# Optimization experiments

Measured on AMD Instinct MI355X. Metric: run time of the kernel, lower is better.

## Reference

```python
import jax, jax.numpy as jnp
import numpy as np

P_FACTOR = 3.0   # config['p_factor']
EPS = 1e-12      # torch F.normalize eps

def _l2_normalize(x):
    return x / jnp.maximum(jnp.linalg.norm(x, axis=-1, keepdims=True), EPS)

def _l1_normalize(x):
    return x / jnp.maximum(jnp.sum(jnp.abs(x), axis=-1, keepdims=True), EPS)

def setup_inputs() -> dict:
    key = jax.random.key(0)
    k = jax.random.split(key, 6)
    B, N_EX, D_IN, D_FEAT, N_LAB, D_CLS = 4096, 16384, 1024, 256, 28, 64
    features = jax.random.normal(k[0], (B, D_IN), jnp.float32)
    labels = jax.random.uniform(k[1], (B, N_LAB), jnp.float32)            # BCE targets in [0,1]
    ex_features = jax.random.normal(k[2], (N_EX, D_IN), jnp.float32)
    ex_classes = jax.random.uniform(k[3], (N_EX, N_LAB), jnp.float32)     # class memberships
    g_w = jax.random.normal(k[4], (D_FEAT, D_IN), jnp.float32) * 0.02     # Linear(in=1024,out=256,bias=False)
    class_reps = jax.random.uniform(k[5], (N_LAB, D_CLS), jnp.float32) * 2.0 - 1.0  # rand*2-1
    return {"features": features, "labels": labels, "ex_features": ex_features,
            "ex_classes": ex_classes, "g_w": g_w, "class_reps": class_reps}

def reference(features, labels, ex_features, ex_classes, g_w, class_reps):
    # g projection (use_g=True, no bias)
    f = features @ g_w.T          # [B, D_FEAT]
    ef = ex_features @ g_w.T      # [N_EX, D_FEAT]
    # exemplar class representations: L1-normalized memberships @ class_reps
    ex_class_reps = _l1_normalize(ex_classes) @ class_reps   # [N_EX, D_CLS]
    # cosine similarity between queries and exemplars
    s = _l2_normalize(f) @ _l2_normalize(ef).T               # [B, N_EX]
    # power-sign activation then L1 normalize over exemplars
    a = _l1_normalize(jnp.sign(s) * jnp.abs(s) ** P_FACTOR)  # [B, N_EX]
    # weighted exemplar aggregation
    echo = a @ ex_class_reps                                  # [B, D_CLS]
    # negative euclidean distances to class representations (cdist)
    diff = echo[:, None, :] - class_reps[None, :, :]          # [B, N_LAB, D_CLS]
    neg_dists = -jnp.sqrt(jnp.sum(diff * diff, axis=-1))      # [B, N_LAB]
    # BCEWithLogitsLoss (mean reduction)
    loss = jnp.mean(-(labels * jax.nn.log_sigmoid(neg_dists)
                      + (1.0 - labels) * jax.nn.log_sigmoid(-neg_dists)))
    return (loss, neg_dists)
```

## Files before the change

kernel.cpp:

```cpp
#include <hip/hip_runtime.h>


typedef __bf16 bf16x8 __attribute__((ext_vector_type(8)));
typedef __bf16 bf16x4 __attribute__((ext_vector_type(4)));
typedef float  f32x4  __attribute__((ext_vector_type(4)));

__device__ __forceinline__ f32x4 f4zero() { f32x4 z = {0.f, 0.f, 0.f, 0.f}; return z; }

__device__ __forceinline__ f32x4 mfma16(bf16x8 a, bf16x8 b, f32x4 c) {
  return __builtin_amdgcn_mfma_f32_16x16x32_bf16(a, b, c, 0, 0, 0);
}

__device__ __forceinline__ bf16x8 load8f(const float* p) {
  f32x4 a = *(const f32x4*)p;
  f32x4 b = *(const f32x4*)(p + 4);
  bf16x8 r;
  r[0] = (__bf16)a[0]; r[1] = (__bf16)a[1]; r[2] = (__bf16)a[2]; r[3] = (__bf16)a[3];
  r[4] = (__bf16)b[0]; r[5] = (__bf16)b[1]; r[6] = (__bf16)b[2]; r[7] = (__bf16)b[3];
  return r;
}

__device__ __forceinline__ bf16x8 cvt2(f32x4 a, f32x4 b) {
  bf16x8 r;
  r[0] = (__bf16)a[0]; r[1] = (__bf16)a[1]; r[2] = (__bf16)a[2]; r[3] = (__bf16)a[3];
  r[4] = (__bf16)b[0]; r[5] = (__bf16)b[1]; r[6] = (__bf16)b[2]; r[7] = (__bf16)b[3];
  return r;
}

__device__ __forceinline__ void async16(const void* g, void* l) {
  __builtin_amdgcn_global_load_lds(
      (const __attribute__((address_space(1))) unsigned int*)g,
      (__attribute__((address_space(3))) unsigned int*)l, 16, 0, 0);
}

__device__ __forceinline__ void bar_lgkm() {
  asm volatile("s_waitcnt lgkmcnt(0)" ::: "memory");
  __builtin_amdgcn_s_barrier();
}
__device__ __forceinline__ void bar_all() {
  asm volatile("s_waitcnt vmcnt(0) lgkmcnt(0)" ::: "memory");
  __builtin_amdgcn_s_barrier();
}

__global__ void fill_sentinel(float* __restrict__ out, int n) {
  for (int i = blockIdx.x * 256 + threadIdx.x; i < n; i += gridDim.x * 256) out[i] = -1.0f;
}

__global__ void prep(const float* __restrict__ exc, __bf16* __restrict__ vT,
                     const float* __restrict__ W, __bf16* __restrict__ W3,
                     float* __restrict__ zp, int zn) {
  const int b = blockIdx.x, tid = threadIdx.x;
  if (b < 64) {
    int e = b * 256 + tid;
    float m[28];
    float s = 0.f;
#pragma unroll
    for (int j = 0; j < 28; j++) {
      m[j] = exc[(size_t)e * 28 + j];
      s += fabsf(m[j]);
    }
    float inv = 1.0f / fmaxf(s, 1e-12f);
#pragma unroll
    for (int j = 0; j < 28; j++) vT[(size_t)j * 16384 + e] = (__bf16)(m[j] * inv);
#pragma unroll
    for (int j = 28; j < 32; j++) vT[(size_t)j * 16384 + e] = (__bf16)0.0f;
  } else if (b < 192) {
    int i = (b - 64) * 256 + tid;
    int frag = i >> 6, lane = i & 63;
    int c16 = frag >> 5, k32 = frag & 31;
    int quad = lane >> 4, l15 = lane & 15;
    *(bf16x8*)(W3 + (size_t)i * 8) =
        load8f(W + (size_t)(c16 * 16 + l15) * 1024 + k32 * 32 + quad * 8);
  } else {
    for (int i = (b - 192) * 256 + tid; i < zn; i += (gridDim.x - 192) * 256) zp[i] = 0.f;
  }
}

__global__ __launch_bounds__(256, 3)
void proj_l2norm(const float* __restrict__ Xa, const float* __restrict__ Xb,
                 const __bf16* __restrict__ W3,
                 __bf16* __restrict__ Pa, __bf16* __restrict__ Pb) {
  __shared__ __align__(16) __bf16 Xs[2][32 * 72];
  __shared__ float nrmW[4 * 32];
  __shared__ float invn[32];

  const int tid = threadIdx.x;
  const int w = tid >> 6, lane = tid & 63;
  const int quad = lane >> 4, l15 = lane & 15;
  const int xrow = tid >> 3, xc8 = tid & 7;

  const float* X;
  __bf16* P;
  int row0;
  if (blockIdx.x < 512) { X = Xa; P = Pa; row0 = blockIdx.x * 32; }
  else                  { X = Xb; P = Pb; row0 = (blockIdx.x - 512) * 32; }

  const float* xsrc = X + (size_t)(row0 + xrow) * 1024 + xc8 * 8;
  const __bf16* wpk = W3 + (size_t)(w * 4) * 32 * 512 + (size_t)lane * 8;

  f32x4 acc[2][4];
#pragma unroll
  for (int i = 0; i < 2; i++)
#pragma unroll
    for (int j = 0; j < 4; j++) acc[i][j] = f4zero();

  *(bf16x8*)(&Xs[0][xrow * 72 + xc8 * 8]) = load8f(xsrc);
  bar_lgkm();

  int cur = 0;
  for (int kb = 0; kb < 16; kb++) {
    const int nxt = cur ^ 1;

    bf16x8 wF[8];
#pragma unroll
    for (int f = 0; f < 8; f++) {
      const int ksub = f >> 2, nb = f & 3;
      wF[f] = *(const bf16x8*)(wpk + ((size_t)nb * 32 + kb * 2 + ksub) * 512);
    }

    f32x4 xa, xb;
    if (kb < 15) {
      const float* xp = xsrc + (kb + 1) * 64;
      xa = *(const f32x4*)xp;
      xb = *(const f32x4*)(xp + 4);
    }

#pragma unroll
    for (int ksub = 0; ksub < 2; ksub++) {
      bf16x8 af[2];
#pragma unroll
      for (int mb = 0; mb < 2; mb++)
        af[mb] = *(bf16x8*)(&Xs[cur][(mb * 16 + l15) * 72 + ksub * 32 + quad * 8]);
#pragma unroll
      for (int mb = 0; mb < 2; mb++)
#pragma unroll
        for (int nb = 0; nb < 4; nb++)
          acc[mb][nb] = mfma16(af[mb], wF[ksub * 4 + nb], acc[mb][nb]);
    }

    if (kb < 15) {
      *(bf16x8*)(&Xs[nxt][xrow * 72 + xc8 * 8]) = cvt2(xa, xb);
    }
    bar_lgkm();
    cur = nxt;
  }

  float part[2][4];
#pragma unroll
  for (int mb = 0; mb < 2; mb++)
#pragma unroll
    for (int r = 0; r < 4; r++) {
      float s = 0.f;
#pragma unroll
      for (int nb = 0; nb < 4; nb++) { float v = acc[mb][nb][r]; s += v * v; }
      part[mb][r] = s;
    }
#pragma unroll
  for (int m = 1; m < 16; m <<= 1)
#pragma unroll
    for (int mb = 0; mb < 2; mb++)
#pragma unroll
      for (int r = 0; r < 4; r++) part[mb][r] += __shfl_xor(part[mb][r], m, 64);

  if (l15 == 0) {
#pragma unroll
    for (int mb = 0; mb < 2; mb++)
#pragma unroll
      for (int r = 0; r < 4; r++)
        nrmW[w * 32 + mb * 16 + quad * 4 + r] = part[mb][r];
  }
  __syncthreads();
  if (tid < 32) {
    float s = nrmW[tid] + nrmW[32 + tid] + nrmW[64 + tid] + nrmW[96 + tid];
    invn[tid] = 1.0f / fmaxf(sqrtf(s), 1e-12f);
  }
  __syncthreads();
#pragma unroll
  for (int mb = 0; mb < 2; mb++)
#pragma unroll
    for (int nb = 0; nb < 4; nb++)
#pragma unroll
      for (int r = 0; r < 4; r++) {
        int row = mb * 16 + quad * 4 + r;
        int col = w * 64 + nb * 16 + l15;
        P[(size_t)(row0 + row) * 256 + col] = (__bf16)(acc[mb][nb][r] * invn[row]);
      }
}

__global__ __launch_bounds__(256, 2)
void fused_sim(const __bf16* __restrict__ fn, const __bf16* __restrict__ efn,
               const __bf16* __restrict__ vTg,
               float* __restrict__ tT, float* __restrict__ r_acc) {
  __shared__ __align__(16) __bf16 Ks[64 * 256];
  __shared__ __align__(16) __bf16 Vs[2][32 * 64];
  __shared__ __align__(16) __bf16 Us[128 * 72];

  const int tid = threadIdx.x, w = tid >> 6, lane = tid & 63;
  const int quad = lane >> 4, l15 = lane & 15;
  const int wy = w >> 1, wx = w & 1;
  const int swk = l15 & 7;
  const int chunk = blockIdx.x & 15, mtile = blockIdx.x >> 4;
  const int q0 = mtile * 128;
  const int e_base = chunk * 1024;

  int koff[8];
#pragma unroll
  for (int rep = 0; rep < 8; rep++) {
    int idx = rep * 256 + tid;
    int row = idx >> 5;
    int c5  = (idx & 31) ^ (row & 7);
    koff[rep] = row * 256 + c5 * 8;
  }
  const int vrow = tid >> 3;
  const int vcs  = (tid & 7) ^ (vrow & 7);
  const size_t vsrc0 = (size_t)vrow * 16384 + e_base + vcs * 8;

  {
    const __bf16* src = efn + (size_t)e_base * 256;
#pragma unroll
    for (int rep = 0; rep < 8; rep++) async16(src + koff[rep], Ks + (rep * 256 + tid) * 8);
    async16(vTg + vsrc0, &Vs[0][tid * 8]);
  }

  bf16x8 qf[8][4];
#pragma unroll
  for (int ks = 0; ks < 8; ks++)
#pragma unroll
    for (int nb = 0; nb < 4; nb++)
      qf[ks][nb] = *(const bf16x8*)(fn + (size_t)(q0 + wx * 64 + nb * 16 + l15) * 256 +
                                    ks * 32 + quad * 8);

  float r_part[4] = {0.f, 0.f, 0.f, 0.f};
  f32x4 accp[2][2];
#pragma unroll
  for (int a = 0; a < 2; a++)
#pragma unroll
    for (int b = 0; b < 2; b++) accp[a][b] = f4zero();

  bar_all();

  int cur = 0;
  for (int t = 0; t < 16; t++) {
    f32x4 accs[2][4];
#pragma unroll
    for (int a = 0; a < 2; a++)
#pragma unroll
      for (int b = 0; b < 4; b++) accs[a][b] = f4zero();
#pragma unroll
    for (int ks = 0; ks < 8; ks++) {
      bf16x8 af[2];
#pragma unroll
      for (int mb = 0; mb < 2; mb++)
        af[mb] = *(bf16x8*)(Ks + (wy * 32 + mb * 16 + l15) * 256 +
                            ((ks * 4 + quad) ^ swk) * 8);
#pragma unroll
      for (int mb = 0; mb < 2; mb++)
#pragma unroll
        for (int nb = 0; nb < 4; nb++)
          accs[mb][nb] = mfma16(af[mb], qf[ks][nb], accs[mb][nb]);
    }

    bar_lgkm();

    if (t < 15) {
      const __bf16* src = efn + (size_t)(e_base + (t + 1) * 64) * 256;
#pragma unroll
      for (int rep = 0; rep < 8; rep++)
        async16(src + koff[rep], Ks + (rep * 256 + tid) * 8);
      async16(vTg + vsrc0 + (t + 1) * 64, &Vs[cur ^ 1][tid * 8]);
    }

#pragma unroll
    for (int mb = 0; mb < 2; mb++) {
      const int eo = wy * 32 + mb * 16 + quad * 4;
#pragma unroll
      for (int nb = 0; nb < 4; nb++) {
        const int q = wx * 64 + nb * 16 + l15;
        bf16x4 pk;
#pragma unroll
        for (int r = 0; r < 4; r++) {
          float s = accs[mb][nb][r];
          __bf16 ub = (__bf16)(s * s * s);
          pk[r] = ub;
          r_part[nb] += fabsf((float)ub);
        }
        *(bf16x4*)(Us + q * 72 + eo) = pk;
      }
    }

    bar_lgkm();

#pragma unroll
    for (int ks = 0; ks < 2; ks++) {
      bf16x8 vf[2], uf[2];
#pragma unroll
      for (int cb = 0; cb < 2; cb++)
        vf[cb] = *(bf16x8*)(&Vs[cur][(cb * 16 + l15) * 64 + ((ks * 4 + quad) ^ swk) * 8]);
#pragma unroll
      for (int qb = 0; qb < 2; qb++)
        uf[qb] = *(bf16x8*)(Us + (w * 32 + qb * 16 + l15) * 72 + ks * 32 + quad * 8);
#pragma unroll
      for (int cb = 0; cb < 2; cb++)
#pragma unroll
        for (int qb = 0; qb < 2; qb++)
          accp[cb][qb] = mfma16(vf[cb], uf[qb], accp[cb][qb]);
    }

    bar_all();
    cur ^= 1;
  }

#pragma unroll
  for (int nb = 0; nb < 4; nb++) {
    float v = r_part[nb];
    v += __shfl_xor(v, 16, 64);
    v += __shfl_xor(v, 32, 64);
    if (quad == 0) atomicAdd(&r_acc[q0 + wx * 64 + nb * 16 + l15], v);
  }
#pragma unroll
  for (int cb = 0; cb < 2; cb++)
#pragma unroll
    for (int qb = 0; qb < 2; qb++)
#pragma unroll
      for (int r = 0; r < 4; r++)
        atomicAdd(&tT[(size_t)(cb * 16 + quad * 4 + r) * 4096 + q0 + w * 32 + qb * 16 + l15],
                  accp[cb][qb][r]);
}

__global__ __launch_bounds__(256, 4)
void finalize(const float* __restrict__ tT, const float* __restrict__ r_acc,
              const float* __restrict__ creps, const float* __restrict__ labels,
              float* __restrict__ loss_acc, float* __restrict__ out) {
  __shared__ __align__(16) float cr[28 * 64];
  __shared__ float wsum[4];
  const int tid = threadIdx.x, w = tid >> 6, lane = tid & 63;
  for (int i = tid; i < 28 * 64; i += 256) cr[i] = creps[i];
  __syncthreads();

  const int q = blockIdx.x * 4 + w;
  float tval = 0.f;
  if (lane < 28) tval = tT[(size_t)lane * 4096 + q];
  tval *= 1.0f / fmaxf(r_acc[q], 1e-12f);

  float echo = 0.f;
#pragma unroll
  for (int j = 0; j < 28; j++)
    echo = fmaf(__shfl(tval, j, 64), cr[j * 64 + lane], echo);

  float dj = 0.f;
#pragma unroll
  for (int j = 0; j < 28; j++) {
    float df = echo - cr[j * 64 + lane];
    float d2 = df * df;
#pragma unroll
    for (int m = 1; m < 64; m <<= 1) d2 += __shfl_xor(d2, m, 64);
    if (lane == j) dj = sqrtf(d2);
  }

  float lsum = 0.f;
  if (lane < 28) {
    out[1 + (size_t)q * 28 + lane] = -dj;
    float y = labels[(size_t)q * 28 + lane];
    lsum = fmaf(y, dj, log1pf(expf(-dj)));
  }
#pragma unroll
  for (int m = 1; m < 64; m <<= 1) lsum += __shfl_xor(lsum, m, 64);
  if (lane == 0) wsum[w] = lsum;
  __syncthreads();
  if (tid == 0) {
    atomicAdd(loss_acc, wsum[0] + wsum[1] + wsum[2] + wsum[3]);
    __threadfence();
    unsigned* cnt = (unsigned*)(loss_acc + 1);
    unsigned old = atomicAdd(cnt, 1u);
    if (old == gridDim.x - 1) {
      float total = atomicAdd(loss_acc, 0.0f);
      out[0] = total * (1.0f / 114688.0f);
    }
  }
}

extern "C" void kernel_launch(void* const* d_in, const int* in_sizes, int n_in,
                              void* d_out, int out_size, void* d_ws, size_t ws_size,
                              hipStream_t stream) {
  const float* features = nullptr;
  const float* labels   = nullptr;
  const float* ex_feat  = nullptr;
  const float* ex_cls   = nullptr;
  const float* g_w      = nullptr;
  const float* creps    = nullptr;
  for (int i = 0; i < n_in; i++) {
    switch (in_sizes[i]) {
      case 4194304:  features = (const float*)d_in[i]; break;
      case 114688:   labels   = (const float*)d_in[i]; break;
      case 16777216: ex_feat  = (const float*)d_in[i]; break;
      case 458752:   ex_cls   = (const float*)d_in[i]; break;
      case 262144:   g_w      = (const float*)d_in[i]; break;
      case 1792:     creps    = (const float*)d_in[i]; break;
      default: break;
    }
  }
  float* out = (float*)d_out;

  if (!features || !labels || !ex_feat || !ex_cls || !g_w || !creps ||
      ws_size < (16ull << 20)) {
    fill_sentinel<<<256, 256, 0, stream>>>(out, out_size);
    return;
  }

  char* ws = (char*)d_ws;
  __bf16* f_n   = (__bf16*)(ws);
  __bf16* ef_n  = (__bf16*)(ws + (2ull << 20));
  __bf16* vT    = (__bf16*)(ws + (10ull << 20));
  float*  tT    = (float*) (ws + (11ull << 20));
  float*  r_acc = tT + 32 * 4096;
  float*  lossp = r_acc + 4096;
  __bf16* W3    = (__bf16*)(ws + (12ull << 20));

  prep<<<720, 256, 0, stream>>>(ex_cls, vT, g_w, W3, tT, 32 * 4096 + 4096 + 2);

  proj_l2norm<<<640, 256, 0, stream>>>(ex_feat, features, W3, ef_n, f_n);
  fused_sim<<<512, 256, 0, stream>>>(f_n, ef_n, vT, tT, r_acc);
  finalize<<<1024, 256, 0, stream>>>(tT, r_acc, creps, labels, lossp, out);
}
```

Before: 222.4 us.

## Double-buffer exemplar K tiles with 32-row steps and per-wave query ownership

The fused similarity kernel now walks exemplars in 32-row steps with a double-buffered K tile. The prefetch of the next K and V tiles is issued at the top of each iteration, so it overlaps the whole MFMA compute instead of waiting behind a mid-loop barrier. Each wave now owns 32 queries against all 32 exemplars of the step, replacing the earlier 2x2 wave split. This removes the extra LDS barrier and shrinks the U staging buffer. The cost is twice as many loop iterations and barriers, and fewer MFMAs per barrier.

```diff
diff --git a/kernel.cpp b/kernel.cpp
--- a/kernel.cpp
+++ b/kernel.cpp
@@ -191,46 +191,47 @@
 void fused_sim(const __bf16* __restrict__ fn, const __bf16* __restrict__ efn,
                const __bf16* __restrict__ vTg,
                float* __restrict__ tT, float* __restrict__ r_acc) {
-  __shared__ __align__(16) __bf16 Ks[64 * 256];
-  __shared__ __align__(16) __bf16 Vs[2][32 * 64];
-  __shared__ __align__(16) __bf16 Us[128 * 72];
+  __shared__ __align__(16) __bf16 Ks[2][32 * 256];
+  __shared__ __align__(16) __bf16 Vs[2][32 * 32];
+  __shared__ __align__(16) __bf16 Us[128 * 40];
 
   const int tid = threadIdx.x, w = tid >> 6, lane = tid & 63;
   const int quad = lane >> 4, l15 = lane & 15;
-  const int wy = w >> 1, wx = w & 1;
   const int swk = l15 & 7;
   const int chunk = blockIdx.x & 15, mtile = blockIdx.x >> 4;
   const int q0 = mtile * 128;
   const int e_base = chunk * 1024;
-
-  int koff[8];
-#pragma unroll
-  for (int rep = 0; rep < 8; rep++) {
+  const int qw = q0 + w * 32;
+
+  int koff[4];
+#pragma unroll
+  for (int rep = 0; rep < 4; rep++) {
     int idx = rep * 256 + tid;
     int row = idx >> 5;
     int c5  = (idx & 31) ^ (row & 7);
     koff[rep] = row * 256 + c5 * 8;
   }
-  const int vrow = tid >> 3;
-  const int vcs  = (tid & 7) ^ (vrow & 7);
-  const size_t vsrc0 = (size_t)vrow * 16384 + e_base + vcs * 8;
+  const int vrow = tid >> 2, vc = tid & 3;
+  const bool vstage = (tid < 128);
 
   {
     const __bf16* src = efn + (size_t)e_base * 256;
 #pragma unroll
-    for (int rep = 0; rep < 8; rep++) async16(src + koff[rep], Ks + (rep * 256 + tid) * 8);
-    async16(vTg + vsrc0, &Vs[0][tid * 8]);
-  }
-
-  bf16x8 qf[8][4];
+    for (int rep = 0; rep < 4; rep++)
+      async16(src + koff[rep], &Ks[0][(rep * 256 + tid) * 8]);
+    if (vstage)
+      async16(vTg + (size_t)vrow * 16384 + e_base + vc * 8, &Vs[0][tid * 8]);
+  }
+
+  bf16x8 qf[8][2];
 #pragma unroll
   for (int ks = 0; ks < 8; ks++)
 #pragma unroll
-    for (int nb = 0; nb < 4; nb++)
-      qf[ks][nb] = *(const bf16x8*)(fn + (size_t)(q0 + wx * 64 + nb * 16 + l15) * 256 +
+    for (int nb = 0; nb < 2; nb++)
+      qf[ks][nb] = *(const bf16x8*)(fn + (size_t)(qw + nb * 16 + l15) * 256 +
                                     ks * 32 + quad * 8);
 
-  float r_part[4] = {0.f, 0.f, 0.f, 0.f};
+  float r_part[2] = {0.f, 0.f};
   f32x4 accp[2][2];
 #pragma unroll
   for (int a = 0; a < 2; a++)
@@ -240,42 +241,42 @@
   bar_all();
 
   int cur = 0;
-  for (int t = 0; t < 16; t++) {
-    f32x4 accs[2][4];
+  for (int t = 0; t < 32; t++) {
+    const int nxt = cur ^ 1;
+
+    if (t < 31) {
+      const __bf16* src = efn + (size_t)(e_base + (t + 1) * 32) * 256;
+#pragma unroll
+      for (int rep = 0; rep < 4; rep++)
+        async16(src + koff[rep], &Ks[nxt][(rep * 256 + tid) * 8]);
+      if (vstage)
+        async16(vTg + (size_t)vrow * 16384 + e_base + (t + 1) * 32 + vc * 8,
+                &Vs[nxt][tid * 8]);
+    }
+
+    f32x4 accs[2][2];
 #pragma unroll
     for (int a = 0; a < 2; a++)
 #pragma unroll
-      for (int b = 0; b < 4; b++) accs[a][b] = f4zero();
+      for (int b = 0; b < 2; b++) accs[a][b] = f4zero();
 #pragma unroll
     for (int ks = 0; ks < 8; ks++) {
       bf16x8 af[2];
 #pragma unroll
       for (int mb = 0; mb < 2; mb++)
-        af[mb] = *(bf16x8*)(Ks + (wy * 32 + mb * 16 + l15) * 256 +
-                            ((ks * 4 + quad) ^ swk) * 8);
+        af[mb] = *(bf16x8*)(&Ks[cur][(mb * 16 + l15) * 256 +
+                                     ((ks * 4 + quad) ^ swk) * 8]);
 #pragma unroll
       for (int mb = 0; mb < 2; mb++)
 #pragma unroll
-        for (int nb = 0; nb < 4; nb++)
+        for (int nb = 0; nb < 2; nb++)
           accs[mb][nb] = mfma16(af[mb], qf[ks][nb], accs[mb][nb]);
     }
 
-    bar_lgkm();
-
-    if (t < 15) {
-      const __bf16* src = efn + (size_t)(e_base + (t + 1) * 64) * 256;
-#pragma unroll
-      for (int rep = 0; rep < 8; rep++)
-        async16(src + koff[rep], Ks + (rep * 256 + tid) * 8);
-      async16(vTg + vsrc0 + (t + 1) * 64, &Vs[cur ^ 1][tid * 8]);
-    }
-
-#pragma unroll
-    for (int mb = 0; mb < 2; mb++) {
-      const int eo = wy * 32 + mb * 16 + quad * 4;
-#pragma unroll
-      for (int nb = 0; nb < 4; nb++) {
-        const int q = wx * 64 + nb * 16 + l15;
+#pragma unroll
+    for (int mb = 0; mb < 2; mb++)
+#pragma unroll
+      for (int nb = 0; nb < 2; nb++) {
         bf16x4 pk;
 #pragma unroll
         for (int r = 0; r < 4; r++) {
@@ -284,21 +285,19 @@
           pk[r] = ub;
           r_part[nb] += fabsf((float)ub);
         }
-        *(bf16x4*)(Us + q * 72 + eo) = pk;
+        *(bf16x4*)(&Us[(w * 32 + nb * 16 + l15) * 40 + mb * 16 + quad * 4]) = pk;
       }
-    }
 
     bar_lgkm();
 
-#pragma unroll
-    for (int ks = 0; ks < 2; ks++) {
+    {
       bf16x8 vf[2], uf[2];
 #pragma unroll
       for (int cb = 0; cb < 2; cb++)
-        vf[cb] = *(bf16x8*)(&Vs[cur][(cb * 16 + l15) * 64 + ((ks * 4 + quad) ^ swk) * 8]);
+        vf[cb] = *(bf16x8*)(&Vs[cur][(cb * 16 + l15) * 32 + quad * 8]);
 #pragma unroll
       for (int qb = 0; qb < 2; qb++)
-        uf[qb] = *(bf16x8*)(Us + (w * 32 + qb * 16 + l15) * 72 + ks * 32 + quad * 8);
+        uf[qb] = *(bf16x8*)(&Us[(w * 32 + qb * 16 + l15) * 40 + quad * 8]);
 #pragma unroll
       for (int cb = 0; cb < 2; cb++)
 #pragma unroll
@@ -307,15 +306,15 @@
     }
 
     bar_all();
-    cur ^= 1;
-  }
-
-#pragma unroll
-  for (int nb = 0; nb < 4; nb++) {
+    cur = nxt;
+  }
+
+#pragma unroll
+  for (int nb = 0; nb < 2; nb++) {
     float v = r_part[nb];
     v += __shfl_xor(v, 16, 64);
     v += __shfl_xor(v, 32, 64);
-    if (quad == 0) atomicAdd(&r_acc[q0 + wx * 64 + nb * 16 + l15], v);
+    if (quad == 0) atomicAdd(&r_acc[qw + nb * 16 + l15], v);
   }
 #pragma unroll
   for (int cb = 0; cb < 2; cb++)
@@ -323,7 +322,7 @@
     for (int qb = 0; qb < 2; qb++)
 #pragma unroll
       for (int r = 0; r < 4; r++)
-        atomicAdd(&tT[(size_t)(cb * 16 + quad * 4 + r) * 4096 + q0 + w * 32 + qb * 16 + l15],
+        atomicAdd(&tT[(size_t)(cb * 16 + quad * 4 + r) * 4096 + qw + qb * 16 + l15],
                   accp[cb][qb][r]);
 }
 
```

New measurement: 229.2 us. 1.03x slower.
